# Performance work log

Measured on AMD Instinct MI355X. Metric: run time of the kernel, lower is better.

## Reference

```python
import jax, jax.numpy as jnp
import numpy as np

EMBED_DIM = 512
NUM_HEADS = 8
EDGE_THRESHOLD = 0.1


def setup_inputs() -> dict:
    key = jax.random.key(0)
    ks = jax.random.split(key, 8)
    E, H = EMBED_DIM, NUM_HEADS
    B, S = 2, 2048
    s = 0.02
    return {
        'hidden_states': jax.random.normal(ks[0], (B, S, E), jnp.float32),
        'Wq': jax.random.normal(ks[1], (E, E), jnp.float32) * s,
        'bq': jnp.zeros((E,), jnp.float32),
        'Wk': jax.random.normal(ks[2], (E, E), jnp.float32) * s,
        'bk': jnp.zeros((E,), jnp.float32),
        'Wv': jax.random.normal(ks[3], (E, E), jnp.float32) * s,
        'bv': jnp.zeros((E,), jnp.float32),
        'Wm1': jax.random.normal(ks[4], (E, E + H), jnp.float32) * s,
        'bm1': jnp.zeros((E,), jnp.float32),
        'Wm2': jax.random.normal(ks[5], (E, E), jnp.float32) * s,
        'bm2': jnp.zeros((E,), jnp.float32),
        'Wo': jax.random.normal(ks[6], (E, E), jnp.float32) * s,
        'bo': jnp.zeros((E,), jnp.float32),
    }


def reference(hidden_states, Wq, bq, Wk, bk, Wv, bv, Wm1, bm1, Wm2, bm2, Wo, bo):
    B, S, E = hidden_states.shape
    H = NUM_HEADS
    hd = E // H
    scale = 1.0 / np.sqrt(hd).astype(np.float32)
    x = hidden_states

    q = (x @ Wq.T + bq).reshape(B, S, H, hd)
    k = (x @ Wk.T + bk).reshape(B, S, H, hd)
    v = (x @ Wv.T + bv)  # kept flat [B,S,E]

    # edge weights: softmax over source nodes j, per head
    scores = jnp.einsum('bihd,bjhd->bijh', q, k) * scale  # [B,S,S,H]
    edge_weights = jax.nn.softmax(scores, axis=2)
    ew_mean = edge_weights.mean(axis=-1)  # [B,S,S]
    adjacency = (ew_mean > EDGE_THRESHOLD).astype(x.dtype)

    # message passing: mean of (edge-weighted features) over adjacent neighbors
    masked_w = ew_mean * adjacency
    aggregated = jnp.einsum('bij,bjd->bid', masked_w, x)
    num_neighbors = jnp.clip(adjacency.sum(axis=-1, keepdims=True), 1.0, None)
    messages = aggregated / num_neighbors

    # gated MLP over [node_features ; mean edge features]
    edge_features = edge_weights.mean(axis=2)  # [B,S,H]
    combined = jnp.concatenate([x, edge_features], axis=-1)
    h = jax.nn.gelu(combined @ Wm1.T + bm1, approximate=False)
    updated = (h @ Wm2.T + bm2) + messages

    attended = jnp.einsum('bij,bjd->bid', ew_mean, v)
    out = (updated + attended) @ Wo.T + bo  # dropout p=0 -> identity
    return out
```

## Files before the change

kernel.cpp:

```cpp
#include <hip/hip_runtime.h>
#include <hip/hip_bf16.h>
#include <math.h>

#define BB 2
#define SS 2048
#define EE 512
#define HH 8
#define NN (BB*SS)
#define JC1 8
#define JCP 4

typedef __attribute__((ext_vector_type(8))) short short8;
typedef __attribute__((ext_vector_type(4))) float f32x4;

__device__ __forceinline__ float b2f(short v){
    return __uint_as_float(((unsigned)(unsigned short)v) << 16);
}
__device__ __forceinline__ unsigned f2bf(float f){
    unsigned u = __float_as_uint(f);
    u += 0x7fffu + ((u >> 16) & 1u);
    return u >> 16;
}
__device__ __forceinline__ void stage16_f32(const float* __restrict__ src,
                                            __hip_bfloat16* dst){
    const float4 f0 = *reinterpret_cast<const float4*>(src);
    const float4 f1 = *reinterpret_cast<const float4*>(src + 4);
    const float4 f2 = *reinterpret_cast<const float4*>(src + 8);
    const float4 f3 = *reinterpret_cast<const float4*>(src + 12);
    uint4 o0, o1;
    o0.x = f2bf(f0.x) | (f2bf(f0.y) << 16);
    o0.y = f2bf(f0.z) | (f2bf(f0.w) << 16);
    o0.z = f2bf(f1.x) | (f2bf(f1.y) << 16);
    o0.w = f2bf(f1.z) | (f2bf(f1.w) << 16);
    o1.x = f2bf(f2.x) | (f2bf(f2.y) << 16);
    o1.y = f2bf(f2.z) | (f2bf(f2.w) << 16);
    o1.z = f2bf(f3.x) | (f2bf(f3.y) << 16);
    o1.w = f2bf(f3.z) | (f2bf(f3.w) << 16);
    *reinterpret_cast<uint4*>(dst) = o0;
    *reinterpret_cast<uint4*>(dst + 8) = o1;
}
__device__ __forceinline__ void stage16_b16(const __hip_bfloat16* __restrict__ src,
                                            __hip_bfloat16* dst){
    const uint4* s = reinterpret_cast<const uint4*>(src);
    uint4* d = reinterpret_cast<uint4*>(dst);
    d[0] = s[0]; d[1] = s[1];
}

__global__ void conv_bf16(
    const float* s0, const float* s1, const float* s2, const float* s3,
    const float* s4, const float* s5, const float* s6,
    __hip_bfloat16* d0, __hip_bfloat16* d1, __hip_bfloat16* d2, __hip_bfloat16* d3,
    __hip_bfloat16* d4, __hip_bfloat16* d5, __hip_bfloat16* d6)
{
    const int which = blockIdx.y;
    const float* s; __hip_bfloat16* d; int n;
    switch (which) {
        case 0: s = s0; d = d0; n = 2097152; break;
        case 1: s = s1; d = d1; n = 262144; break;
        case 2: s = s2; d = d2; n = 262144; break;
        case 3: s = s3; d = d3; n = 262144; break;
        case 4: s = s4; d = d4; n = 266240; break;
        case 5: s = s5; d = d5; n = 262144; break;
        default: s = s6; d = d6; n = 262144; break;
    }
    const int base = (blockIdx.x * 256 + threadIdx.x) * 4;
    if (base >= n) return;
    const float4 f = *reinterpret_cast<const float4*>(s + base);
    uint2 o;
    o.x = f2bf(f.x) | (f2bf(f.y) << 16);
    o.y = f2bf(f.z) | (f2bf(f.w) << 16);
    *reinterpret_cast<uint2*>(d + base) = o;
}

template<int B16>
__global__ __launch_bounds__(256) void qkv_gemm(
    const void* __restrict__ x,
    const void* __restrict__ Wq, const float* __restrict__ bq,
    const void* __restrict__ Wk, const float* __restrict__ bk,
    const void* __restrict__ Wv, const float* __restrict__ bv,
    __hip_bfloat16* __restrict__ qb,
    __hip_bfloat16* __restrict__ kb,
    __hip_bfloat16* __restrict__ vT)
{
    __shared__ __hip_bfloat16 As[64][72];
    __shared__ __hip_bfloat16 Bs[64][72];
    const int tid = threadIdx.x;
    const int which = blockIdx.x >> 3;
    const int col0 = (blockIdx.x & 7) * 64;
    const int row0 = blockIdx.y * 64;
    const int wv = tid >> 6, lane = tid & 63, quad = lane >> 4, m16 = lane & 15;
    const int sr = tid >> 2;
    const int sc = (tid & 3) * 16;
    const void* W    = (which == 0) ? Wq : (which == 1) ? Wk : Wv;
    const float* bias = (which == 0) ? bq : (which == 1) ? bk : bv;

    f32x4 acc[4];
    #pragma unroll
    for (int nt = 0; nt < 4; ++nt) acc[nt] = (f32x4){0.f, 0.f, 0.f, 0.f};

    for (int k0 = 0; k0 < 512; k0 += 64) {
        if (B16) {
            stage16_b16((const __hip_bfloat16*)x + (size_t)(row0 + sr) * EE + k0 + sc, &As[sr][sc]);
            stage16_b16((const __hip_bfloat16*)W + (size_t)(col0 + sr) * EE + k0 + sc, &Bs[sr][sc]);
        } else {
            stage16_f32((const float*)x + (size_t)(row0 + sr) * EE + k0 + sc, &As[sr][sc]);
            stage16_f32((const float*)W + (size_t)(col0 + sr) * EE + k0 + sc, &Bs[sr][sc]);
        }
        __syncthreads();
        #pragma unroll
        for (int ks = 0; ks < 2; ++ks) {
            const short8 a = *reinterpret_cast<const short8*>(
                &As[wv * 16 + m16][ks * 32 + quad * 8]);
            #pragma unroll
            for (int nt = 0; nt < 4; ++nt) {
                const short8 b = *reinterpret_cast<const short8*>(
                    &Bs[nt * 16 + m16][ks * 32 + quad * 8]);
                acc[nt] = __builtin_amdgcn_mfma_f32_16x16x32_bf16(a, b, acc[nt], 0, 0, 0);
            }
        }
        __syncthreads();
    }

    if (which == 2) {
        #pragma unroll
        for (int nt = 0; nt < 4; ++nt) {
            const float bb = bias[col0 + nt * 16 + m16];
            #pragma unroll
            for (int r = 0; r < 4; ++r)
                Bs[wv * 16 + quad * 4 + r][nt * 16 + m16] =
                    __float2bfloat16(acc[nt][r] + bb);
        }
        __syncthreads();
        const int bb2 = row0 >> 11;
        const int j0 = row0 & (SS - 1);
        const int er = tid >> 2;
        const int js = (tid & 3) * 16;
        unsigned pk[8];
        #pragma unroll
        for (int p = 0; p < 8; ++p) {
            const unsigned lo = *reinterpret_cast<const unsigned short*>(&Bs[js + 2*p][er]);
            const unsigned hi = *reinterpret_cast<const unsigned short*>(&Bs[js + 2*p + 1][er]);
            pk[p] = lo | (hi << 16);
        }
        uint4 s0; s0.x = pk[0]; s0.y = pk[1]; s0.z = pk[2]; s0.w = pk[3];
        uint4 s1; s1.x = pk[4]; s1.y = pk[5]; s1.z = pk[6]; s1.w = pk[7];
        __hip_bfloat16* dst = vT + ((size_t)(bb2 * EE + col0 + er)) * SS + j0 + js;
        *reinterpret_cast<uint4*>(dst) = s0;
        *reinterpret_cast<uint4*>(dst + 8) = s1;
    } else {
        __hip_bfloat16* C = (which == 0) ? qb : kb;
        #pragma unroll
        for (int nt = 0; nt < 4; ++nt) {
            const int gn = col0 + nt * 16 + m16;
            const float bb = bias[gn];
            #pragma unroll
            for (int r = 0; r < 4; ++r) {
                const int gm = row0 + wv * 16 + quad * 4 + r;
                C[(size_t)gm * EE + gn] = __float2bfloat16(acc[nt][r] + bb);
            }
        }
    }
}

template<int MODE, int AB16, int WB16, int CF32>
__global__ __launch_bounds__(256) void gemm_bt(
    const void* __restrict__ Av,
    const void* __restrict__ Wv_,
    const float* __restrict__ bias,
    void* __restrict__ Cv,
    int ldb)
{
    __shared__ __hip_bfloat16 As[64][72];
    __shared__ __hip_bfloat16 Bs[64][72];
    const int tid = threadIdx.x;
    const int col0 = blockIdx.x * 64;
    const int row0 = blockIdx.y * 64;
    const int wv = tid >> 6, lane = tid & 63, quad = lane >> 4, m16 = lane & 15;
    const int sr = tid >> 2;
    const int sc = (tid & 3) * 16;

    f32x4 acc[4];
    #pragma unroll
    for (int nt = 0; nt < 4; ++nt) acc[nt] = (f32x4){0.f, 0.f, 0.f, 0.f};

    for (int k0 = 0; k0 < 512; k0 += 64) {
        if (AB16)
            stage16_b16((const __hip_bfloat16*)Av + (size_t)(row0 + sr) * EE + k0 + sc, &As[sr][sc]);
        else
            stage16_f32((const float*)Av + (size_t)(row0 + sr) * EE + k0 + sc, &As[sr][sc]);
        if (WB16)
            stage16_b16((const __hip_bfloat16*)Wv_ + (size_t)(col0 + sr) * ldb + k0 + sc, &Bs[sr][sc]);
        else
            stage16_f32((const float*)Wv_ + (size_t)(col0 + sr) * ldb + k0 + sc, &Bs[sr][sc]);
        __syncthreads();
        #pragma unroll
        for (int ks = 0; ks < 2; ++ks) {
            const short8 a = *reinterpret_cast<const short8*>(
                &As[wv * 16 + m16][ks * 32 + quad * 8]);
            #pragma unroll
            for (int nt = 0; nt < 4; ++nt) {
                const short8 b = *reinterpret_cast<const short8*>(
                    &Bs[nt * 16 + m16][ks * 32 + quad * 8]);
                acc[nt] = __builtin_amdgcn_mfma_f32_16x16x32_bf16(a, b, acc[nt], 0, 0, 0);
            }
        }
        __syncthreads();
    }

    #pragma unroll
    for (int nt = 0; nt < 4; ++nt) {
        const int gn = col0 + nt * 16 + m16;
        float bb = bias[gn];
        if (MODE == 1) {
            float ts = 0.f;
            #pragma unroll
            for (int h = 0; h < 8; ++h) {
                const size_t wi = (size_t)gn * ldb + 512 + h;
                ts += WB16 ? (float)((const __hip_bfloat16*)Wv_)[wi]
                           : ((const float*)Wv_)[wi];
            }
            bb += ts * (1.0f / (float)SS);
        }
        #pragma unroll
        for (int r = 0; r < 4; ++r) {
            const int gm = row0 + wv * 16 + quad * 4 + r;
            const size_t ci = (size_t)gm * EE + gn;
            float c = acc[nt][r] + bb;
            if (MODE == 1) c = 0.5f * c * (1.0f + erff(c * 0.70710678118654752f));
            if (MODE == 2) c += (float)((const __hip_bfloat16*)Cv)[ci];
            if (CF32) ((float*)Cv)[ci] = c;
            else      ((__hip_bfloat16*)Cv)[ci] = __float2bfloat16(c);
        }
    }
}

__global__ __launch_bounds__(256) void attn_denoms(
    const __hip_bfloat16* __restrict__ qws,
    const __hip_bfloat16* __restrict__ kws,
    float* __restrict__ dnP,
    int* __restrict__ cntI)
{
    __shared__ __hip_bfloat16 KL[16][520];
    const int tid = threadIdx.x;
    const int wv = tid >> 6, lane = tid & 63, quad = lane >> 4, m16 = lane & 15;
    const int jc = blockIdx.x;
    const int it = blockIdx.y;
    const int b  = blockIdx.z;
    const size_t g0 = (size_t)b * SS + it * 64;
    const size_t gb = (size_t)b * SS;
    const float scale = 0.125f;

    if (jc == 0 && tid < 64) cntI[g0 + tid] = 0;

    short8 aq[HH][2];
    #pragma unroll
    for (int h = 0; h < HH; ++h)
        #pragma unroll
        for (int ks = 0; ks < 2; ++ks)
            aq[h][ks] = *reinterpret_cast<const short8*>(
                qws + (g0 + wv * 16 + m16) * EE + h * 64 + ks * 32 + quad * 8);

    float dph[HH][4];
    #pragma unroll
    for (int h = 0; h < HH; ++h)
        #pragma unroll
        for (int r = 0; r < 4; ++r) dph[h][r] = 0.f;

    const int srow = tid >> 4, scol = (tid & 15) * 32;
    for (int jt = 0; jt < 16; ++jt) {
        const int j0 = jc * 256 + jt * 16;
        const uint4* src = reinterpret_cast<const uint4*>(
            kws + (gb + j0 + srow) * EE + scol);
        uint4* dst = reinterpret_cast<uint4*>(&KL[srow][scol]);
        dst[0] = src[0]; dst[1] = src[1]; dst[2] = src[2]; dst[3] = src[3];
        __syncthreads();
        #pragma unroll
        for (int h = 0; h < HH; ++h) {
            const short8 b0 = *reinterpret_cast<const short8*>(&KL[m16][h * 64 + quad * 8]);
            const short8 b1 = *reinterpret_cast<const short8*>(&KL[m16][h * 64 + 32 + quad * 8]);
            f32x4 c = {0.f, 0.f, 0.f, 0.f};
            c = __builtin_amdgcn_mfma_f32_16x16x32_bf16(aq[h][0], b0, c, 0, 0, 0);
            c = __builtin_amdgcn_mfma_f32_16x16x32_bf16(aq[h][1], b1, c, 0, 0, 0);
            #pragma unroll
            for (int r = 0; r < 4; ++r) dph[h][r] += __expf(c[r] * scale);
        }
        __syncthreads();
    }

    #pragma unroll
    for (int h = 0; h < HH; ++h)
        #pragma unroll
        for (int off = 1; off <= 8; off <<= 1)
            #pragma unroll
            for (int r = 0; r < 4; ++r) dph[h][r] += __shfl_xor(dph[h][r], off, 64);
    if (m16 == 0) {
        const size_t i = (size_t)it * 64 + wv * 16 + quad * 4;
        #pragma unroll
        for (int h = 0; h < HH; ++h)
            #pragma unroll
            for (int r = 0; r < 4; ++r)
                dnP[((size_t)(jc * BB + b) * SS + i + r) * HH + h] = dph[h][r];
    }
}

__global__ __launch_bounds__(256, 2) void attn_ewpv(
    const __hip_bfloat16* __restrict__ qws,
    const __hip_bfloat16* __restrict__ kws,
    const __hip_bfloat16* __restrict__ vTg,
    const float* __restrict__ dnP,
    int* __restrict__ cntI,
    int* __restrict__ slotJ,
    float* __restrict__ slotW,
    __hip_bfloat16* __restrict__ pvP)
{
    __shared__ __hip_bfloat16 KL[32][520];
    __shared__ __hip_bfloat16 VL[512][40];
    __shared__ __hip_bfloat16 ewT[32][40];
    __shared__ float invd[HH][32];
    const int tid = threadIdx.x;
    const int wv = tid >> 6, lane = tid & 63, quad = lane >> 4, m16 = lane & 15;
    const int jc = blockIdx.x;
    const int it = blockIdx.y;
    const int b  = blockIdx.z;
    const size_t gb = (size_t)b * SS;
    const size_t g0 = gb + it * 32;
    const int ih = wv & 1;
    const int jh = wv >> 1;

    {
        const int h = tid >> 5, i = tid & 31;
        float s = 0.f;
        #pragma unroll
        for (int c = 0; c < JC1; ++c)
            s += dnP[((size_t)(c * BB + b) * SS + it * 32 + i) * HH + h];
        invd[h][i] = 0.125f / s;
    }

    short8 aq[HH][2];
    #pragma unroll
    for (int h = 0; h < HH; ++h)
        #pragma unroll
        for (int ks = 0; ks < 2; ++ks)
            aq[h][ks] = *reinterpret_cast<const short8*>(
                qws + (g0 + ih * 16 + m16) * EE + h * 64 + ks * 32 + quad * 8);

    f32x4 acc[2][8];
    #pragma unroll
    for (int mf = 0; mf < 2; ++mf)
        #pragma unroll
        for (int nf = 0; nf < 8; ++nf) acc[mf][nf] = (f32x4){0.f, 0.f, 0.f, 0.f};

    const int krow = tid >> 4, kcol = (tid & 15) * 32;
    const int vrow = tid >> 2, vcol = (tid & 3) * 8;
    __syncthreads();

    for (int st = 0; st < 16; ++st) {
        const int j0 = jc * 512 + st * 32;
        #pragma unroll
        for (int rr = 0; rr < 2; ++rr) {
            const uint4* src = reinterpret_cast<const uint4*>(
                kws + (gb + j0 + rr * 16 + krow) * EE + kcol);
            uint4* dst = reinterpret_cast<uint4*>(&KL[rr * 16 + krow][kcol]);
            dst[0] = src[0]; dst[1] = src[1]; dst[2] = src[2]; dst[3] = src[3];
        }
        #pragma unroll
        for (int p = 0; p < 8; ++p)
            *reinterpret_cast<uint4*>(&VL[p * 64 + vrow][vcol]) =
                *reinterpret_cast<const uint4*>(
                    vTg + ((size_t)b * EE + p * 64 + vrow) * SS + j0 + vcol);
        __syncthreads();

        float wsum[4] = {0.f, 0.f, 0.f, 0.f};
        #pragma unroll
        for (int h = 0; h < HH; ++h) {
            const short8 b0 = *reinterpret_cast<const short8*>(
                &KL[jh * 16 + m16][h * 64 + quad * 8]);
            const short8 b1 = *reinterpret_cast<const short8*>(
                &KL[jh * 16 + m16][h * 64 + 32 + quad * 8]);
            f32x4 c = {0.f, 0.f, 0.f, 0.f};
            c = __builtin_amdgcn_mfma_f32_16x16x32_bf16(aq[h][0], b0, c, 0, 0, 0);
            c = __builtin_amdgcn_mfma_f32_16x16x32_bf16(aq[h][1], b1, c, 0, 0, 0);
            #pragma unroll
            for (int r = 0; r < 4; ++r)
                wsum[r] += __expf(c[r] * 0.125f) * invd[h][ih * 16 + quad * 4 + r];
        }
        #pragma unroll
        for (int r = 0; r < 4; ++r) {
            const __hip_bfloat16 wb = __float2bfloat16(wsum[r]);
            ewT[ih * 16 + quad * 4 + r][jh * 16 + m16] = wb;
            if ((float)wb > 0.1f) {
                const int li = ih * 16 + quad * 4 + r;
                const int idx = atomicAdd(&cntI[g0 + li], 1);
                if (idx < 16) {
                    slotJ[((size_t)g0 + li) * 16 + idx] = j0 + jh * 16 + m16;
                    slotW[((size_t)g0 + li) * 16 + idx] = (float)wb;
                }
            }
        }
        __syncthreads();

        {
            const short8 a0 = *reinterpret_cast<const short8*>(&ewT[m16][quad * 8]);
            const short8 a1 = *reinterpret_cast<const short8*>(&ewT[16 + m16][quad * 8]);
            #pragma unroll
            for (int nf = 0; nf < 8; ++nf) {
                const short8 bb = *reinterpret_cast<const short8*>(
                    &VL[wv * 128 + nf * 16 + m16][quad * 8]);
                acc[0][nf] = __builtin_amdgcn_mfma_f32_16x16x32_bf16(a0, bb, acc[0][nf], 0, 0, 0);
                acc[1][nf] = __builtin_amdgcn_mfma_f32_16x16x32_bf16(a1, bb, acc[1][nf], 0, 0, 0);
            }
        }
        __syncthreads();
    }

    #pragma unroll
    for (int mf = 0; mf < 2; ++mf)
        #pragma unroll
        for (int nf = 0; nf < 8; ++nf)
            #pragma unroll
            for (int r = 0; r < 4; ++r)
                KL[mf * 16 + quad * 4 + r][wv * 128 + nf * 16 + m16] =
                    __float2bfloat16(acc[mf][nf][r]);
    __syncthreads();
    const int orow = tid >> 3;
    const int oc = (tid & 7) * 64;
    const uint4* s = reinterpret_cast<const uint4*>(&KL[orow][oc]);
    uint4* d = reinterpret_cast<uint4*>(
        pvP + ((size_t)jc * NN + g0 + orow) * EE + oc);
    #pragma unroll
    for (int q = 0; q < 8; ++q) d[q] = s[q];
}

__global__ __launch_bounds__(256) void pv_combine(
    const __hip_bfloat16* __restrict__ pvP,
    const int* __restrict__ cntI,
    const int* __restrict__ slotJ,
    const float* __restrict__ slotW,
    const float* __restrict__ x,
    __hip_bfloat16* __restrict__ u1out)
{
    const int tid = threadIdx.x;
    const int row = blockIdx.x * 4 + (tid >> 6);
    const int e0 = (tid & 63) * 8;
    float s[8] = {0.f, 0.f, 0.f, 0.f, 0.f, 0.f, 0.f, 0.f};
    #pragma unroll
    for (int c = 0; c < JCP; ++c) {
        const short8 v = *reinterpret_cast<const short8*>(
            pvP + ((size_t)c * NN + row) * EE + e0);
        #pragma unroll
        for (int k = 0; k < 8; ++k) s[k] += b2f(v[k]);
    }
    const int cn = cntI[row];
    if (cn > 0) {
        const float inv = 1.f / (float)cn;
        const int ns = cn < 16 ? cn : 16;
        const int b = row >> 11;
        for (int t = 0; t < ns; ++t) {
            const int j = slotJ[(size_t)row * 16 + t];
            const float w = slotW[(size_t)row * 16 + t] * inv;
            const float* xr = x + ((size_t)b * SS + j) * EE + e0;
            #pragma unroll
            for (int k = 0; k < 8; ++k) s[k] += w * xr[k];
        }
    }
    short8 o;
    #pragma unroll
    for (int k = 0; k < 8; ++k) o[k] = (short)f2bf(s[k]);
    *reinterpret_cast<short8*>(u1out + (size_t)row * EE + e0) = o;
}

extern "C" void kernel_launch(void* const* d_in, const int* in_sizes, int n_in,
                              void* d_out, int out_size, void* d_ws, size_t ws_size,
                              hipStream_t stream)
{
    const float* x   = (const float*)d_in[0];
    const float* Wq  = (const float*)d_in[1];
    const float* bq  = (const float*)d_in[2];
    const float* Wk  = (const float*)d_in[3];
    const float* bk  = (const float*)d_in[4];
    const float* Wv  = (const float*)d_in[5];
    const float* bv  = (const float*)d_in[6];
    const float* Wm1 = (const float*)d_in[7];
    const float* bm1 = (const float*)d_in[8];
    const float* Wm2 = (const float*)d_in[9];
    const float* bm2 = (const float*)d_in[10];
    const float* Wo  = (const float*)d_in[11];
    const float* bo  = (const float*)d_in[12];

    char* ws = (char*)d_ws;
    const size_t MB = 1024 * 1024;
    __hip_bfloat16* qb = (__hip_bfloat16*)(ws + 0);
    __hip_bfloat16* kb = (__hip_bfloat16*)(ws + 4*MB);
    __hip_bfloat16* vT = (__hip_bfloat16*)(ws + 8*MB);
    __hip_bfloat16* pvP = (__hip_bfloat16*)(ws + 12*MB);
    float* dnP = (float*)(ws + 28*MB);
    int*   cntI = (int*)(ws + 29*MB);
    int*   slotJ = (int*)(ws + 29*MB + 64*1024);
    float* slotW = (float*)(ws + 29*MB + 384*1024);
    const bool EXT = (ws_size >= 38 * MB);
    __hip_bfloat16* xb   = (__hip_bfloat16*)(ws + 30*MB);
    __hip_bfloat16* wqb  = (__hip_bfloat16*)(ws + 34*MB);
    __hip_bfloat16* wkb  = (__hip_bfloat16*)(ws + 34*MB + 512*1024);
    __hip_bfloat16* wvb  = (__hip_bfloat16*)(ws + 35*MB);
    __hip_bfloat16* wm1b = (__hip_bfloat16*)(ws + 35*MB + 512*1024);
    __hip_bfloat16* wm2b = (__hip_bfloat16*)(ws + 36*MB + 256*1024);
    __hip_bfloat16* wob  = (__hip_bfloat16*)(ws + 36*MB + 768*1024);

    dim3 blk(256, 1, 1);
    dim3 gg(EE / 64, NN / 64, 1);

    if (EXT) {
        conv_bf16<<<dim3(2048, 7, 1), blk, 0, stream>>>(
            x, Wq, Wk, Wv, Wm1, Wm2, Wo, xb, wqb, wkb, wvb, wm1b, wm2b, wob);
        qkv_gemm<1><<<dim3(24, NN / 64, 1), blk, 0, stream>>>(
            xb, wqb, bq, wkb, bk, wvb, bv, qb, kb, vT);
    } else {
        qkv_gemm<0><<<dim3(24, NN / 64, 1), blk, 0, stream>>>(
            x, Wq, bq, Wk, bk, Wv, bv, qb, kb, vT);
    }
    attn_denoms<<<dim3(JC1, SS / 64, BB), blk, 0, stream>>>(qb, kb, dnP, cntI);
    attn_ewpv<<<dim3(JCP, SS / 32, BB), blk, 0, stream>>>(
        qb, kb, vT, dnP, cntI, slotJ, slotW, pvP);
    pv_combine<<<dim3(NN / 4, 1, 1), blk, 0, stream>>>(
        pvP, cntI, slotJ, slotW, x, qb);
    if (EXT) {
        gemm_bt<1,1,1,0><<<gg, blk, 0, stream>>>(xb, wm1b, bm1, kb, EE + HH);
        gemm_bt<2,1,1,0><<<gg, blk, 0, stream>>>(kb, wm2b, bm2, qb, EE);
        gemm_bt<0,1,1,1><<<gg, blk, 0, stream>>>(qb, wob, bo, d_out, EE);
    } else {
        gemm_bt<1,0,0,0><<<gg, blk, 0, stream>>>(x, Wm1, bm1, kb, EE + HH);
        gemm_bt<2,1,0,0><<<gg, blk, 0, stream>>>(kb, Wm2, bm2, qb, EE);
        gemm_bt<0,1,0,1><<<gg, blk, 0, stream>>>(qb, Wo, bo, d_out, EE);
    }
}
```

Measured before the change: 236.0 us.

## Double-buffer K tiles in LDS and load V fragments directly from global

Both attention kernels now double-buffer the K tile in shared memory. The next tile is prefetched into registers while MFMAs run on the current one, which allows one barrier per iteration to be dropped. In attn_ewpv the V tile is no longer staged through LDS; each wave reads its V fragments straight from global memory into registers, removing the VL buffer and its barrier. This adds register pressure and uncoalesced strided global V reads in exchange for fewer syncs and less LDS traffic.

```diff
diff --git a/kernel.cpp b/kernel.cpp
--- a/kernel.cpp
+++ b/kernel.cpp
@@ -240,7 +240,7 @@
     float* __restrict__ dnP,
     int* __restrict__ cntI)
 {
-    __shared__ __hip_bfloat16 KL[16][520];
+    __shared__ __hip_bfloat16 KL[2][16][520];
     const int tid = threadIdx.x;
     const int wv = tid >> 6, lane = tid & 63, quad = lane >> 4, m16 = lane & 15;
     const int jc = blockIdx.x;
@@ -248,7 +248,6 @@
     const int b  = blockIdx.z;
     const size_t g0 = (size_t)b * SS + it * 64;
     const size_t gb = (size_t)b * SS;
-    const float scale = 0.125f;
 
     if (jc == 0 && tid < 64) cntI[g0 + tid] = 0;
 
@@ -267,24 +266,35 @@
         for (int r = 0; r < 4; ++r) dph[h][r] = 0.f;
 
     const int srow = tid >> 4, scol = (tid & 15) * 32;
+    {
+        const uint4* src = reinterpret_cast<const uint4*>(
+            kws + (gb + jc * 256 + srow) * EE + scol);
+        uint4* dst = reinterpret_cast<uint4*>(&KL[0][srow][scol]);
+        dst[0] = src[0]; dst[1] = src[1]; dst[2] = src[2]; dst[3] = src[3];
+    }
+
     for (int jt = 0; jt < 16; ++jt) {
-        const int j0 = jc * 256 + jt * 16;
-        const uint4* src = reinterpret_cast<const uint4*>(
-            kws + (gb + j0 + srow) * EE + scol);
-        uint4* dst = reinterpret_cast<uint4*>(&KL[srow][scol]);
-        dst[0] = src[0]; dst[1] = src[1]; dst[2] = src[2]; dst[3] = src[3];
-        __syncthreads();
+        __syncthreads();
+        uint4 kr[4];
+        if (jt + 1 < 16) {
+            const uint4* src = reinterpret_cast<const uint4*>(
+                kws + (gb + jc * 256 + (jt + 1) * 16 + srow) * EE + scol);
+            kr[0] = src[0]; kr[1] = src[1]; kr[2] = src[2]; kr[3] = src[3];
+        }
         #pragma unroll
         for (int h = 0; h < HH; ++h) {
-            const short8 b0 = *reinterpret_cast<const short8*>(&KL[m16][h * 64 + quad * 8]);
-            const short8 b1 = *reinterpret_cast<const short8*>(&KL[m16][h * 64 + 32 + quad * 8]);
+            const short8 b0 = *reinterpret_cast<const short8*>(&KL[jt & 1][m16][h * 64 + quad * 8]);
+            const short8 b1 = *reinterpret_cast<const short8*>(&KL[jt & 1][m16][h * 64 + 32 + quad * 8]);
             f32x4 c = {0.f, 0.f, 0.f, 0.f};
             c = __builtin_amdgcn_mfma_f32_16x16x32_bf16(aq[h][0], b0, c, 0, 0, 0);
             c = __builtin_amdgcn_mfma_f32_16x16x32_bf16(aq[h][1], b1, c, 0, 0, 0);
             #pragma unroll
-            for (int r = 0; r < 4; ++r) dph[h][r] += __expf(c[r] * scale);
-        }
-        __syncthreads();
+            for (int r = 0; r < 4; ++r) dph[h][r] += __expf(c[r] * 0.125f);
+        }
+        if (jt + 1 < 16) {
+            uint4* dst = reinterpret_cast<uint4*>(&KL[(jt + 1) & 1][srow][scol]);
+            dst[0] = kr[0]; dst[1] = kr[1]; dst[2] = kr[2]; dst[3] = kr[3];
+        }
     }
 
     #pragma unroll
@@ -313,8 +323,7 @@
     float* __restrict__ slotW,
     __hip_bfloat16* __restrict__ pvP)
 {
-    __shared__ __hip_bfloat16 KL[32][520];
-    __shared__ __hip_bfloat16 VL[512][40];
+    __shared__ __hip_bfloat16 KL[2][32][520];
     __shared__ __hip_bfloat16 ewT[32][40];
     __shared__ float invd[HH][32];
     const int tid = threadIdx.x;
@@ -351,32 +360,43 @@
         for (int nf = 0; nf < 8; ++nf) acc[mf][nf] = (f32x4){0.f, 0.f, 0.f, 0.f};
 
     const int krow = tid >> 4, kcol = (tid & 15) * 32;
-    const int vrow = tid >> 2, vcol = (tid & 3) * 8;
-    __syncthreads();
+    {
+        #pragma unroll
+        for (int rr = 0; rr < 2; ++rr) {
+            const uint4* src = reinterpret_cast<const uint4*>(
+                kws + (gb + jc * 512 + rr * 16 + krow) * EE + kcol);
+            uint4* dst = reinterpret_cast<uint4*>(&KL[0][rr * 16 + krow][kcol]);
+            dst[0] = src[0]; dst[1] = src[1]; dst[2] = src[2]; dst[3] = src[3];
+        }
+    }
+    const __hip_bfloat16* vrow0 = vTg + ((size_t)b * EE + wv * 128 + m16) * SS + quad * 8;
 
     for (int st = 0; st < 16; ++st) {
         const int j0 = jc * 512 + st * 32;
-        #pragma unroll
-        for (int rr = 0; rr < 2; ++rr) {
-            const uint4* src = reinterpret_cast<const uint4*>(
-                kws + (gb + j0 + rr * 16 + krow) * EE + kcol);
-            uint4* dst = reinterpret_cast<uint4*>(&KL[rr * 16 + krow][kcol]);
-            dst[0] = src[0]; dst[1] = src[1]; dst[2] = src[2]; dst[3] = src[3];
-        }
-        #pragma unroll
-        for (int p = 0; p < 8; ++p)
-            *reinterpret_cast<uint4*>(&VL[p * 64 + vrow][vcol]) =
-                *reinterpret_cast<const uint4*>(
-                    vTg + ((size_t)b * EE + p * 64 + vrow) * SS + j0 + vcol);
-        __syncthreads();
+        __syncthreads();
+
+        short8 vb[8];
+        #pragma unroll
+        for (int nf = 0; nf < 8; ++nf)
+            vb[nf] = *reinterpret_cast<const short8*>(vrow0 + (size_t)(nf * 16) * SS + j0);
+        uint4 kr[8];
+        if (st + 1 < 16) {
+            #pragma unroll
+            for (int rr = 0; rr < 2; ++rr) {
+                const uint4* src = reinterpret_cast<const uint4*>(
+                    kws + (gb + j0 + 32 + rr * 16 + krow) * EE + kcol);
+                kr[rr * 4 + 0] = src[0]; kr[rr * 4 + 1] = src[1];
+                kr[rr * 4 + 2] = src[2]; kr[rr * 4 + 3] = src[3];
+            }
+        }
 
         float wsum[4] = {0.f, 0.f, 0.f, 0.f};
         #pragma unroll
         for (int h = 0; h < HH; ++h) {
             const short8 b0 = *reinterpret_cast<const short8*>(
-                &KL[jh * 16 + m16][h * 64 + quad * 8]);
+                &KL[st & 1][jh * 16 + m16][h * 64 + quad * 8]);
             const short8 b1 = *reinterpret_cast<const short8*>(
-                &KL[jh * 16 + m16][h * 64 + 32 + quad * 8]);
+                &KL[st & 1][jh * 16 + m16][h * 64 + 32 + quad * 8]);
             f32x4 c = {0.f, 0.f, 0.f, 0.f};
             c = __builtin_amdgcn_mfma_f32_16x16x32_bf16(aq[h][0], b0, c, 0, 0, 0);
             c = __builtin_amdgcn_mfma_f32_16x16x32_bf16(aq[h][1], b1, c, 0, 0, 0);
@@ -399,18 +419,24 @@
         }
         __syncthreads();
 
+        if (st + 1 < 16) {
+            #pragma unroll
+            for (int rr = 0; rr < 2; ++rr) {
+                uint4* dst = reinterpret_cast<uint4*>(&KL[(st + 1) & 1][rr * 16 + krow][kcol]);
+                dst[0] = kr[rr * 4 + 0]; dst[1] = kr[rr * 4 + 1];
+                dst[2] = kr[rr * 4 + 2]; dst[3] = kr[rr * 4 + 3];
+            }
+        }
+
         {
             const short8 a0 = *reinterpret_cast<const short8*>(&ewT[m16][quad * 8]);
             const short8 a1 = *reinterpret_cast<const short8*>(&ewT[16 + m16][quad * 8]);
             #pragma unroll
             for (int nf = 0; nf < 8; ++nf) {
-                const short8 bb = *reinterpret_cast<const short8*>(
-                    &VL[wv * 128 + nf * 16 + m16][quad * 8]);
-                acc[0][nf] = __builtin_amdgcn_mfma_f32_16x16x32_bf16(a0, bb, acc[0][nf], 0, 0, 0);
-                acc[1][nf] = __builtin_amdgcn_mfma_f32_16x16x32_bf16(a1, bb, acc[1][nf], 0, 0, 0);
-            }
-        }
-        __syncthreads();
+                acc[0][nf] = __builtin_amdgcn_mfma_f32_16x16x32_bf16(a0, vb[nf], acc[0][nf], 0, 0, 0);
+                acc[1][nf] = __builtin_amdgcn_mfma_f32_16x16x32_bf16(a1, vb[nf], acc[1][nf], 0, 0, 0);
+            }
+        }
     }
 
     #pragma unroll
@@ -419,12 +445,12 @@
         for (int nf = 0; nf < 8; ++nf)
             #pragma unroll
             for (int r = 0; r < 4; ++r)
-                KL[mf * 16 + quad * 4 + r][wv * 128 + nf * 16 + m16] =
+                KL[0][mf * 16 + quad * 4 + r][wv * 128 + nf * 16 + m16] =
                     __float2bfloat16(acc[mf][nf][r]);
     __syncthreads();
     const int orow = tid >> 3;
     const int oc = (tid & 7) * 64;
-    const uint4* s = reinterpret_cast<const uint4*>(&KL[orow][oc]);
+    const uint4* s = reinterpret_cast<const uint4*>(&KL[0][orow][oc]);
     uint4* d = reinterpret_cast<uint4*>(
         pvP + ((size_t)jc * NN + g0 + orow) * EE + oc);
     #pragma unroll
```

Measured after the change: 277.2 us. +17.4%, slower.
